# Optimization experiments

Measured on AMD Instinct MI355X. Metric: run time of the kernel, lower is better.

Reference implementation:

```python
import jax, jax.numpy as jnp
import numpy as np

B, T, D, H = 8, 1024, 768, 12
HD = D // H  # head_dim = 64


def setup_inputs() -> dict:
    key = jax.random.key(0)
    ks = jax.random.split(key, 6)
    s = 1.0 / np.sqrt(D)
    return {
        "x": jax.random.normal(ks[0], (B, T, D), dtype=jnp.float32),
        "Wq": jax.random.normal(ks[1], (D, D), dtype=jnp.float32) * s,
        "Wk": jax.random.normal(ks[2], (D, D), dtype=jnp.float32) * s,
        "Wv": jax.random.normal(ks[3], (D, D), dtype=jnp.float32) * s,
        "Wp": jax.random.normal(ks[4], (D, D), dtype=jnp.float32) * s,
        "bp": jnp.zeros((D,), dtype=jnp.float32),
    }


def reference(x, Wq, Wk, Wv, Wp, bp):
    Bx, Tx, Dx = x.shape
    # projections (nn.Linear applies x @ W.T; weights here are stored as [out,in]-equivalent square)
    q = (x @ Wq.T).reshape(Bx, Tx, H, HD).transpose(0, 2, 1, 3)  # [B,H,T,hd]
    k = (x @ Wk.T).reshape(Bx, Tx, H, HD).transpose(0, 2, 1, 3)
    v = (x @ Wv.T).reshape(Bx, Tx, H, HD).transpose(0, 2, 1, 3)
    scores = jnp.einsum("bhqd,bhkd->bhqk", q, k)  # raw QK^T, then mask, then scale (as in source)
    causal = jnp.tril(jnp.ones((Tx, Tx), dtype=bool))
    scores = jnp.where(causal, scores, -jnp.inf)
    weights = jax.nn.softmax(scores / np.sqrt(HD), axis=-1)
    # dropout is identity in eval mode
    ctx = jnp.einsum("bhqk,bhkd->bhqd", weights, v)
    ctx = ctx.transpose(0, 2, 1, 3).reshape(Bx, Tx, Dx)
    return ctx @ Wp.T + bp
```

## Files before the change

kernel.cpp:

```cpp
#include <hip/hip_runtime.h>
#include <math.h>

#define Bsz 8
#define Tsz 1024
#define Dsz 768
#define Hn  12
#define Msz (Bsz*Tsz)
#define NQT (Tsz/64)

typedef __attribute__((ext_vector_type(8))) short bf16x8_t;
typedef __attribute__((ext_vector_type(4))) float f32x4_t;

__device__ __forceinline__ unsigned short f2bf(float f) {
  unsigned u = __builtin_bit_cast(unsigned, f);
  u += 0x7FFFu + ((u >> 16) & 1u);
  return (unsigned short)(u >> 16);
}

__device__ __forceinline__ void gload16(const void* g, const void* l) {
  __builtin_amdgcn_global_load_lds(
      (const __attribute__((address_space(1))) unsigned int*)g,
      (__attribute__((address_space(3))) unsigned int*)l, 16, 0, 0);
}

__global__ __launch_bounds__(256) void cvt_x_kernel(const float* __restrict__ in,
                                                    unsigned short* __restrict__ out) {
  size_t idx = ((size_t)blockIdx.x * 256 + threadIdx.x) * 4;
  float4 v = *(const float4*)(in + idx);
  union { unsigned short u[4]; uint2 w; } t;
  t.u[0] = f2bf(v.x); t.u[1] = f2bf(v.y); t.u[2] = f2bf(v.z); t.u[3] = f2bf(v.w);
  *(uint2*)(out + idx) = t.w;
}

__global__ __launch_bounds__(256) void cvt_w_kernel(
    const float* __restrict__ w0, const float* __restrict__ w1,
    const float* __restrict__ w2, const float* __restrict__ w3,
    unsigned short* __restrict__ o0, unsigned short* __restrict__ o1,
    unsigned short* __restrict__ o2, unsigned short* __restrict__ o3) {
  const float* src; unsigned short* dst;
  switch (blockIdx.y) {
    case 0: src = w0; dst = o0; break;
    case 1: src = w1; dst = o1; break;
    case 2: src = w2; dst = o2; break;
    default: src = w3; dst = o3; break;
  }
  size_t idx = ((size_t)blockIdx.x * 256 + threadIdx.x) * 4;
  float4 v = *(const float4*)(src + idx);
  union { unsigned short u[4]; uint2 w; } t;
  t.u[0] = f2bf(v.x); t.u[1] = f2bf(v.y); t.u[2] = f2bf(v.z); t.u[3] = f2bf(v.w);
  *(uint2*)(dst + idx) = t.w;
}

__global__ __launch_bounds__(256) void gemm_qkv_kernel(
    const unsigned short* __restrict__ X, const unsigned short* __restrict__ Wcat,
    unsigned short* __restrict__ Yq, unsigned short* __restrict__ Yk,
    unsigned short* __restrict__ Yvt) {
  __shared__ __align__(16) unsigned short As[128 * 32];
  __shared__ __align__(16) unsigned short Bs[128 * 32];
  const int tid = threadIdx.x;
  const int w = tid >> 6, lane = tid & 63;
  const int i = lane & 15, g = lane >> 4;
  const int wr = w >> 1, wc = w & 1;
  const int bm = blockIdx.x * 128, bn = blockIdx.y * 128;

  f32x4_t acc[4][4];
  #pragma unroll
  for (int a = 0; a < 4; ++a)
    #pragma unroll
    for (int b2 = 0; b2 < 4; ++b2)
      #pragma unroll
      for (int r = 0; r < 4; ++r) acc[a][b2][r] = 0.f;

  for (int k0 = 0; k0 < Dsz; k0 += 32) {
    __syncthreads();
    #pragma unroll
    for (int j = 0; j < 2; ++j) {
      const int c = 2 * w + j;
      const int row = 16 * c + (lane >> 2);
      const int cb = (lane & 3) * 16;
      const char* ga = (const char*)X + ((size_t)(bm + row) * Dsz + k0) * 2 + cb;
      gload16(ga, (const char*)As + c * 1024);
      const char* gb = (const char*)Wcat + ((size_t)(bn + row) * Dsz + k0) * 2 + cb;
      gload16(gb, (const char*)Bs + c * 1024);
    }
    __syncthreads();
    bf16x8_t af[4], bfr[4];
    #pragma unroll
    for (int f = 0; f < 4; ++f) {
      af[f]  = *(const bf16x8_t*)&As[(64 * wr + 16 * f + i) * 32 + 8 * g];
      bfr[f] = *(const bf16x8_t*)&Bs[(64 * wc + 16 * f + i) * 32 + 8 * g];
    }
    #pragma unroll
    for (int a = 0; a < 4; ++a)
      #pragma unroll
      for (int b2 = 0; b2 < 4; ++b2)
        acc[a][b2] = __builtin_amdgcn_mfma_f32_16x16x32_bf16(af[a], bfr[b2], acc[a][b2], 0, 0, 0);
  }

  const int wsel = blockIdx.y / 6;
  const int nloc = (blockIdx.y % 6) * 128;
  if (wsel < 2) {
    unsigned short* Y = wsel ? Yk : Yq;
    #pragma unroll
    for (int fi = 0; fi < 4; ++fi)
      #pragma unroll
      for (int fj = 0; fj < 4; ++fj) {
        const int n = nloc + 64 * wc + 16 * fj + i;
        #pragma unroll
        for (int r = 0; r < 4; ++r) {
          const int m = bm + 64 * wr + 16 * fi + 4 * g + r;
          Y[(size_t)m * Dsz + n] = f2bf(acc[fi][fj][r]);
        }
      }
  } else {
    #pragma unroll
    for (int fi = 0; fi < 4; ++fi)
      #pragma unroll
      for (int fj = 0; fj < 4; ++fj) {
        const int m0 = bm + 64 * wr + 16 * fi + 4 * g;
        const int bb = m0 >> 10;
        const int t  = m0 & 1023;
        const int n  = nloc + 64 * wc + 16 * fj + i;
        union { unsigned short u[4]; uint2 v; } pk;
        #pragma unroll
        for (int r = 0; r < 4; ++r) pk.u[r] = f2bf(acc[fi][fj][r]);
        *(uint2*)&Yvt[((size_t)(bb * Dsz + n)) * Tsz + t] = pk.v;
      }
  }
}

__global__ __launch_bounds__(256) void gemm_proj_kernel(
    const unsigned short* __restrict__ X, const unsigned short* __restrict__ W,
    const float* __restrict__ bias, float* __restrict__ Y) {
  __shared__ __align__(16) unsigned short As[128 * 32];
  __shared__ __align__(16) unsigned short Bs[128 * 32];
  const int tid = threadIdx.x;
  const int w = tid >> 6, lane = tid & 63;
  const int i = lane & 15, g = lane >> 4;
  const int wr = w >> 1, wc = w & 1;
  const int bm = blockIdx.x * 128, bn = blockIdx.y * 128;

  f32x4_t acc[4][4];
  #pragma unroll
  for (int a = 0; a < 4; ++a)
    #pragma unroll
    for (int b2 = 0; b2 < 4; ++b2)
      #pragma unroll
      for (int r = 0; r < 4; ++r) acc[a][b2][r] = 0.f;

  for (int k0 = 0; k0 < Dsz; k0 += 32) {
    __syncthreads();
    #pragma unroll
    for (int j = 0; j < 2; ++j) {
      const int c = 2 * w + j;
      const int row = 16 * c + (lane >> 2);
      const int cb = (lane & 3) * 16;
      const char* ga = (const char*)X + ((size_t)(bm + row) * Dsz + k0) * 2 + cb;
      gload16(ga, (const char*)As + c * 1024);
      const char* gb = (const char*)W + ((size_t)(bn + row) * Dsz + k0) * 2 + cb;
      gload16(gb, (const char*)Bs + c * 1024);
    }
    __syncthreads();
    bf16x8_t af[4], bfr[4];
    #pragma unroll
    for (int f = 0; f < 4; ++f) {
      af[f]  = *(const bf16x8_t*)&As[(64 * wr + 16 * f + i) * 32 + 8 * g];
      bfr[f] = *(const bf16x8_t*)&Bs[(64 * wc + 16 * f + i) * 32 + 8 * g];
    }
    #pragma unroll
    for (int a = 0; a < 4; ++a)
      #pragma unroll
      for (int b2 = 0; b2 < 4; ++b2)
        acc[a][b2] = __builtin_amdgcn_mfma_f32_16x16x32_bf16(af[a], bfr[b2], acc[a][b2], 0, 0, 0);
  }

  #pragma unroll
  for (int fi = 0; fi < 4; ++fi)
    #pragma unroll
    for (int fj = 0; fj < 4; ++fj) {
      const int n = bn + 64 * wc + 16 * fj + i;
      const float bv = bias[n];
      #pragma unroll
      for (int r = 0; r < 4; ++r) {
        const int m = bm + 64 * wr + 16 * fi + 4 * g + r;
        Y[(size_t)m * Dsz + n] = acc[fi][fj][r] + bv;
      }
    }
}

__global__ __launch_bounds__(256) void attn_mfma_kernel(
    const unsigned short* __restrict__ Qm, const unsigned short* __restrict__ Km,
    const unsigned short* __restrict__ Vt, unsigned short* __restrict__ ctx) {
  __shared__ __align__(16) unsigned short Ks[128 * 64];
  __shared__ __align__(16) unsigned short Vs[64 * 128];
  __shared__ __align__(16) unsigned short Ps[4][16 * 136];
  const int tid = threadIdx.x, w = tid >> 6, lane = tid & 63;
  const int i = lane & 15, g = lane >> 4;
  const int bh = blockIdx.y, b = bh / Hn, h = bh % Hn;
  const int kr8 = lane >> 3;
  const int kb8 = (lane & 7) * 16;
  const int vr4 = lane >> 4;
  const int vb4 = (lane & 15) * 16;

  for (int tsel = 0; tsel < 2; ++tsel) {
    const int qt = tsel ? (NQT - 1 - (int)blockIdx.x) : (int)blockIdx.x;
    const int t0 = qt * 64;

    bf16x8_t qa[2];
    {
      const unsigned short* qp =
          Qm + ((size_t)(b * Tsz + t0 + 16 * w + i) * Dsz + h * 64 + 8 * g);
      qa[0] = *(const bf16x8_t*)qp;
      qa[1] = *(const bf16x8_t*)(qp + 32);
    }

    f32x4_t o[4];
    #pragma unroll
    for (int fd = 0; fd < 4; ++fd)
      #pragma unroll
      for (int r = 0; r < 4; ++r) o[fd][r] = 0.f;
    float mrun[4] = {-3.0e38f, -3.0e38f, -3.0e38f, -3.0e38f};
    float lrun[4] = {0.f, 0.f, 0.f, 0.f};

    const int nt2 = qt / 2 + 1;
    for (int kt2 = 0; kt2 < nt2; ++kt2) {
      const int k0 = kt2 * 128;
      const bool uh = (k0 + 64) <= (t0 + 63);
      const int nfj = uh ? 8 : 4;
      const int nks = uh ? 4 : 2;

      __syncthreads();
      #pragma unroll
      for (int j = 0; j < 4; ++j) {
        const int c = 4 * j + w;
        const int krow = 8 * c + kr8;
        const char* gk = (const char*)Km +
            ((size_t)(b * Tsz + k0 + krow) * Dsz + h * 64) * 2 +
            (kb8 ^ ((kr8 & 7) << 4));
        gload16(gk, (const char*)Ks + c * 1024);
        const int vrow = 4 * c + vr4;
        const char* gv = (const char*)Vt +
            ((size_t)(bh * 64 + vrow) * Tsz + k0) * 2 +
            (vb4 ^ ((vrow & 7) << 4));
        gload16(gv, (const char*)Vs + c * 1024);
      }
      __syncthreads();

      f32x4_t s[8];
      #pragma unroll
      for (int fj = 0; fj < 8; ++fj) {
        if (fj >= nfj) continue;
        #pragma unroll
        for (int r = 0; r < 4; ++r) s[fj][r] = 0.f;
        #pragma unroll
        for (int ks = 0; ks < 2; ++ks) {
          const int R = 16 * fj + i;
          const bf16x8_t kb = *(const bf16x8_t*)((const char*)Ks + R * 128 +
                                                 ((16 * g + 64 * ks) ^ ((R & 7) << 4)));
          s[fj] = __builtin_amdgcn_mfma_f32_16x16x32_bf16(qa[ks], kb, s[fj], 0, 0, 0);
        }
      }

      float mx[4] = {-3.0e38f, -3.0e38f, -3.0e38f, -3.0e38f};
      #pragma unroll
      for (int fj = 0; fj < 8; ++fj) {
        if (fj >= nfj) continue;
        const int kidx = k0 + 16 * fj + i;
        #pragma unroll
        for (int r = 0; r < 4; ++r) {
          float v = s[fj][r] * 0.125f;
          if (kidx > t0 + 16 * w + 4 * g + r) v = -1.0e30f;
          s[fj][r] = v;
          mx[r] = fmaxf(mx[r], v);
        }
      }
      #pragma unroll
      for (int r = 0; r < 4; ++r) {
        mx[r] = fmaxf(mx[r], __shfl_xor(mx[r], 1));
        mx[r] = fmaxf(mx[r], __shfl_xor(mx[r], 2));
        mx[r] = fmaxf(mx[r], __shfl_xor(mx[r], 4));
        mx[r] = fmaxf(mx[r], __shfl_xor(mx[r], 8));
      }
      float fs[4];
      #pragma unroll
      for (int r = 0; r < 4; ++r) {
        const float mn = fmaxf(mrun[r], mx[r]);
        fs[r] = __expf(mrun[r] - mn);
        mrun[r] = mn;
      }
      float rs[4] = {0.f, 0.f, 0.f, 0.f};
      #pragma unroll
      for (int fj = 0; fj < 8; ++fj) {
        if (fj >= nfj) continue;
        #pragma unroll
        for (int r = 0; r < 4; ++r) {
          s[fj][r] = __expf(s[fj][r] - mrun[r]);
          rs[r] += s[fj][r];
        }
      }
      #pragma unroll
      for (int r = 0; r < 4; ++r) {
        rs[r] += __shfl_xor(rs[r], 1);
        rs[r] += __shfl_xor(rs[r], 2);
        rs[r] += __shfl_xor(rs[r], 4);
        rs[r] += __shfl_xor(rs[r], 8);
        lrun[r] = lrun[r] * fs[r] + rs[r];
      }
      #pragma unroll
      for (int fd = 0; fd < 4; ++fd)
        #pragma unroll
        for (int r = 0; r < 4; ++r) o[fd][r] *= fs[r];

      #pragma unroll
      for (int fj = 0; fj < 8; ++fj) {
        if (fj >= nfj) continue;
        #pragma unroll
        for (int r = 0; r < 4; ++r)
          Ps[w][(4 * g + r) * 136 + 16 * fj + i] = f2bf(s[fj][r]);
      }

      #pragma unroll
      for (int ks = 0; ks < 4; ++ks) {
        if (ks >= nks) continue;
        const bf16x8_t pa = *(const bf16x8_t*)&Ps[w][i * 136 + 32 * ks + 8 * g];
        #pragma unroll
        for (int fd = 0; fd < 4; ++fd) {
          const int R = 16 * fd + i;
          const bf16x8_t vb = *(const bf16x8_t*)((const char*)Vs + R * 256 +
                                                 ((16 * g + 64 * ks) ^ ((R & 7) << 4)));
          o[fd] = __builtin_amdgcn_mfma_f32_16x16x32_bf16(pa, vb, o[fd], 0, 0, 0);
        }
      }
    }

    #pragma unroll
    for (int r = 0; r < 4; ++r) {
      const float inv = 1.f / lrun[r];
      const int qidx = t0 + 16 * w + 4 * g + r;
      #pragma unroll
      for (int fd = 0; fd < 4; ++fd)
        ctx[(size_t)(b * Tsz + qidx) * Dsz + h * 64 + 16 * fd + i] =
            f2bf(o[fd][r] * inv);
    }
  }
}

extern "C" void kernel_launch(void* const* d_in, const int* in_sizes, int n_in,
                              void* d_out, int out_size, void* d_ws, size_t ws_size,
                              hipStream_t stream) {
  const float* x  = (const float*)d_in[0];
  const float* Wq = (const float*)d_in[1];
  const float* Wk = (const float*)d_in[2];
  const float* Wv = (const float*)d_in[3];
  const float* Wp = (const float*)d_in[4];
  const float* bp = (const float*)d_in[5];
  float* out = (float*)d_out;

  const size_t md = (size_t)Msz * Dsz;
  const size_t wd = (size_t)Dsz * Dsz;
  unsigned short* xb   = (unsigned short*)d_ws;
  unsigned short* wqb  = xb + md;
  unsigned short* wkb  = wqb + wd;
  unsigned short* wvb  = wkb + wd;
  unsigned short* wpb  = wvb + wd;
  unsigned short* qb   = wpb + wd;
  unsigned short* kb   = qb + md;
  unsigned short* vtb  = kb + md;
  unsigned short* ctxb = vtb + md;

  cvt_x_kernel<<<md / 1024, 256, 0, stream>>>(x, xb);
  cvt_w_kernel<<<dim3(wd / 1024, 4), 256, 0, stream>>>(Wq, Wk, Wv, Wp, wqb, wkb, wvb, wpb);

  gemm_qkv_kernel<<<dim3(Msz / 128, 18), 256, 0, stream>>>(xb, wqb, qb, kb, vtb);

  attn_mfma_kernel<<<dim3(NQT / 2, Bsz * Hn), 256, 0, stream>>>(qb, kb, vtb, ctxb);

  gemm_proj_kernel<<<dim3(Msz / 128, Dsz / 128), 256, 0, stream>>>(ctxb, wpb, bp, out);
}
```

Baseline: 231.5 us.

## Fold softmax scale into Q, use exp2, lazy rescale, alias K/P smem

Folds the 1/sqrt(hd)*log2(e) factor into the Q projection epilogue so the attention kernel can use exp2 without a per-score multiply. The causal mask is applied only on the diagonal tile. The running max and output rescale are updated only when some row's max grows by more than 8 (in log2 units), which skips most rescale work. The P buffer now aliases the K buffer in LDS, which lowers shared memory use (aiding occupancy) but needs an extra barrier per tile. Skipping rescales lets unnormalised values grow by up to 2^8 in fp32/bf16, which the final normalisation absorbs.

Result: no change. 228.9 us (-1.1%).

```diff
diff --git a/kernel.cpp b/kernel.cpp
--- a/kernel.cpp
+++ b/kernel.cpp
@@ -101,6 +101,7 @@
   const int nloc = (blockIdx.y % 6) * 128;
   if (wsel < 2) {
     unsigned short* Y = wsel ? Yk : Yq;
+    const float sc = wsel ? 1.0f : 0.18033688f;
     #pragma unroll
     for (int fi = 0; fi < 4; ++fi)
       #pragma unroll
@@ -109,7 +110,7 @@
         #pragma unroll
         for (int r = 0; r < 4; ++r) {
           const int m = bm + 64 * wr + 16 * fi + 4 * g + r;
-          Y[(size_t)m * Dsz + n] = f2bf(acc[fi][fj][r]);
+          Y[(size_t)m * Dsz + n] = f2bf(acc[fi][fj][r] * sc);
         }
       }
   } else {
@@ -191,9 +192,9 @@
 __global__ __launch_bounds__(256) void attn_mfma_kernel(
     const unsigned short* __restrict__ Qm, const unsigned short* __restrict__ Km,
     const unsigned short* __restrict__ Vt, unsigned short* __restrict__ ctx) {
-  __shared__ __align__(16) unsigned short Ks[128 * 64];
+  __shared__ __align__(16) unsigned short KP[4 * 16 * 136];
   __shared__ __align__(16) unsigned short Vs[64 * 128];
-  __shared__ __align__(16) unsigned short Ps[4][16 * 136];
+  unsigned short* Ks = KP;
   const int tid = threadIdx.x, w = tid >> 6, lane = tid & 63;
   const int i = lane & 15, g = lane >> 4;
   const int bh = blockIdx.y, b = bh / Hn, h = bh % Hn;
@@ -228,6 +229,7 @@
       const bool uh = (k0 + 64) <= (t0 + 63);
       const int nfj = uh ? 8 : 4;
       const int nks = uh ? 4 : 2;
+      const bool dtile = (kt2 == (qt >> 1));
 
       __syncthreads();
       #pragma unroll
@@ -261,18 +263,23 @@
         }
       }
 
+      if (dtile) {
+        #pragma unroll
+        for (int fj = 0; fj < 8; ++fj) {
+          if (fj >= nfj) continue;
+          const int kidx = k0 + 16 * fj + i;
+          #pragma unroll
+          for (int r = 0; r < 4; ++r)
+            if (kidx > t0 + 16 * w + 4 * g + r) s[fj][r] = -1.0e30f;
+        }
+      }
+
       float mx[4] = {-3.0e38f, -3.0e38f, -3.0e38f, -3.0e38f};
       #pragma unroll
       for (int fj = 0; fj < 8; ++fj) {
         if (fj >= nfj) continue;
-        const int kidx = k0 + 16 * fj + i;
-        #pragma unroll
-        for (int r = 0; r < 4; ++r) {
-          float v = s[fj][r] * 0.125f;
-          if (kidx > t0 + 16 * w + 4 * g + r) v = -1.0e30f;
-          s[fj][r] = v;
-          mx[r] = fmaxf(mx[r], v);
-        }
+        #pragma unroll
+        for (int r = 0; r < 4; ++r) mx[r] = fmaxf(mx[r], s[fj][r]);
       }
       #pragma unroll
       for (int r = 0; r < 4; ++r) {
@@ -281,20 +288,29 @@
         mx[r] = fmaxf(mx[r], __shfl_xor(mx[r], 4));
         mx[r] = fmaxf(mx[r], __shfl_xor(mx[r], 8));
       }
-      float fs[4];
-      #pragma unroll
-      for (int r = 0; r < 4; ++r) {
-        const float mn = fmaxf(mrun[r], mx[r]);
-        fs[r] = __expf(mrun[r] - mn);
-        mrun[r] = mn;
-      }
+
+      bool nd = false;
+      #pragma unroll
+      for (int r = 0; r < 4; ++r) nd = nd || (mx[r] > mrun[r] + 8.0f);
+      if (__any(nd)) {
+        #pragma unroll
+        for (int r = 0; r < 4; ++r) {
+          const float mn = fmaxf(mrun[r], mx[r]);
+          const float fs = exp2f(mrun[r] - mn);
+          mrun[r] = mn;
+          lrun[r] *= fs;
+          #pragma unroll
+          for (int fd = 0; fd < 4; ++fd) o[fd][r] *= fs;
+        }
+      }
+
       float rs[4] = {0.f, 0.f, 0.f, 0.f};
       #pragma unroll
       for (int fj = 0; fj < 8; ++fj) {
         if (fj >= nfj) continue;
         #pragma unroll
         for (int r = 0; r < 4; ++r) {
-          s[fj][r] = __expf(s[fj][r] - mrun[r]);
+          s[fj][r] = exp2f(s[fj][r] - mrun[r]);
           rs[r] += s[fj][r];
         }
       }
@@ -304,25 +320,24 @@
         rs[r] += __shfl_xor(rs[r], 2);
         rs[r] += __shfl_xor(rs[r], 4);
         rs[r] += __shfl_xor(rs[r], 8);
-        lrun[r] = lrun[r] * fs[r] + rs[r];
-      }
-      #pragma unroll
-      for (int fd = 0; fd < 4; ++fd)
-        #pragma unroll
-        for (int r = 0; r < 4; ++r) o[fd][r] *= fs[r];
-
+        lrun[r] += rs[r];
+      }
+
+      __syncthreads();
+
+      unsigned short* Pw = KP + w * (16 * 136);
       #pragma unroll
       for (int fj = 0; fj < 8; ++fj) {
         if (fj >= nfj) continue;
         #pragma unroll
         for (int r = 0; r < 4; ++r)
-          Ps[w][(4 * g + r) * 136 + 16 * fj + i] = f2bf(s[fj][r]);
+          Pw[(4 * g + r) * 136 + 16 * fj + i] = f2bf(s[fj][r]);
       }
 
       #pragma unroll
       for (int ks = 0; ks < 4; ++ks) {
         if (ks >= nks) continue;
-        const bf16x8_t pa = *(const bf16x8_t*)&Ps[w][i * 136 + 32 * ks + 8 * g];
+        const bf16x8_t pa = *(const bf16x8_t*)&Pw[i * 136 + 32 * ks + 8 * g];
         #pragma unroll
         for (int fd = 0; fd < 4; ++fd) {
           const int R = 16 * fd + i;
```
